# Kernel tuning notes

Hardware: AMD Instinct MI355X
Metric: run time of the kernel (lower is better)

## Reference

```python
import jax, jax.numpy as jnp
import numpy as np

B, C1, C2, H, W, NH = 16, 256, 256, 64, 64, 8
C = C2 // 2          # hidden dim of retention blocks (c2*e)
HD = C // NH         # head dim
EPS = 1e-5           # torch BatchNorm2d / LayerNorm default eps


def _ln(x, g, b):
    mu = jnp.mean(x, -1, keepdims=True)
    var = jnp.mean((x - mu) ** 2, -1, keepdims=True)
    return (x - mu) * jax.lax.rsqrt(var + EPS) * g + b


def _bn_silu(y, g, b, m, v):
    # inference-mode BatchNorm2d (running stats) + SiLU, channels axis=1
    y = (y - m[:, None, None]) * jax.lax.rsqrt(v + EPS)[:, None, None] * g[:, None, None] + b[:, None, None]
    return jax.nn.silu(y)


def _decay1d(L, dec):
    # RelPos2d.generate_1d_decay: exp(decay_n * |i-j|), shape (NH, L, L)
    idx = jnp.arange(L)
    m = jnp.abs(idx[:, None] - idx[None, :]).astype(jnp.float32)
    return jnp.exp(dec[:, None, None] * m)


def setup_inputs() -> dict:
    key = jax.random.key(0)
    ks = jax.random.split(key, 8)
    s = 0.02
    return {
        'x': jax.random.normal(ks[0], (B, C1, H, W), jnp.float32),
        'cv1_w': jax.random.normal(ks[1], (2 * C, C1), jnp.float32) * s,
        'bn1_g': jnp.ones((2 * C,)), 'bn1_b': jnp.zeros((2 * C,)),
        'bn1_m': jnp.zeros((2 * C,)), 'bn1_v': jnp.ones((2 * C,)),
        'cv2_w': jax.random.normal(ks[2], (C2, 3 * C), jnp.float32) * s,
        'bn2_g': jnp.ones((C2,)), 'bn2_b': jnp.zeros((C2,)),
        'bn2_m': jnp.zeros((C2,)), 'bn2_v': jnp.ones((C2,)),
        'ln1_g': jnp.ones((C,)), 'ln1_b': jnp.zeros((C,)),
        'qkv_w': jax.random.normal(ks[3], (3 * C, C), jnp.float32) * s,
        'qkv_b': jnp.zeros((3 * C,)),
        'proj_w': jax.random.normal(ks[4], (C, C), jnp.float32) * s,
        'proj_b': jnp.zeros((C,)),
        'gamma': jnp.ones((C,)),
        'ln2_g': jnp.ones((C,)), 'ln2_b': jnp.zeros((C,)),
        'ffn_w1': jax.random.normal(ks[5], (2 * C, C), jnp.float32) * s,
        'ffn_b1': jnp.zeros((2 * C,)),
        'ffn_w2': jax.random.normal(ks[6], (C, 2 * C), jnp.float32) * s,
        'ffn_b2': jnp.zeros((C,)),
    }


def reference(x, cv1_w, bn1_g, bn1_b, bn1_m, bn1_v, cv2_w, bn2_g, bn2_b, bn2_m, bn2_v,
              ln1_g, ln1_b, qkv_w, qkv_b, proj_w, proj_b, gamma,
              ln2_g, ln2_b, ffn_w1, ffn_b1, ffn_w2, ffn_b2):
    # RelPos2d: decay per head, initial_value=2, heads_range=4; mode='chunk' -> 1D decays
    dec = jnp.log(1.0 - 2.0 ** (-2.0 - 4.0 * jnp.arange(NH, dtype=jnp.float32) / NH))
    decay_h = _decay1d(H, dec)  # (NH, H, H)
    decay_w = _decay1d(W, dec)  # (NH, W, W)

    # cv1: 1x1 conv + BN + SiLU, then chunk into two halves of C channels
    y = _bn_silu(jnp.einsum('bchw,oc->bohw', x, cv1_w), bn1_g, bn1_b, bn1_m, bn1_v)
    y1, y2 = y[:, :C], y[:, C:]

    # RetBlock on channels-last feature map
    f = jnp.transpose(y2, (0, 2, 3, 1))  # (B,H,W,C)
    res = f
    fn = _ln(f, ln1_g, ln1_b)
    qkv = fn @ qkv_w.T + qkv_b
    q, k, v = jnp.split(qkv, 3, axis=-1)

    def heads(t):
        return jnp.transpose(t.reshape(B, H, W, NH, HD), (0, 3, 1, 2, 4))  # (B,NH,H,W,HD)

    q, k, v = heads(q), heads(k), heads(v)

    # axial retention: row attention with exponential row-decay
    qk_h = jnp.einsum('bnhwc,bnHwc->bnhHw', q, k) * decay_h[None, :, :, :, None]
    out_h = jnp.einsum('bnhHw,bnHwc->bnhwc', qk_h, v)
    # column attention with exponential column-decay
    qk_w = jnp.einsum('bnhwc,bnhWc->bnhwW', q, k) * decay_w[None, :, None, :, :]
    out_w = jnp.einsum('bnhwW,bnhWc->bnhwc', qk_w, v)
    out = 0.5 * (out_h + out_w)
    out = jnp.transpose(out, (0, 2, 3, 1, 4)).reshape(B, H, W, C)

    f = res + (out @ proj_w.T + proj_b) * gamma
    res2 = f
    fn2 = _ln(f, ln2_g, ln2_b)
    h1 = jax.nn.gelu(fn2 @ ffn_w1.T + ffn_b1, approximate=False)
    f = res2 + (h1 @ ffn_w2.T + ffn_b2)

    f = jnp.transpose(f, (0, 3, 1, 2))  # back to (B,C,H,W)
    cat = jnp.concatenate([y1, y2, f], axis=1)  # (B,3C,H,W)
    return _bn_silu(jnp.einsum('bchw,oc->bohw', cat, cv2_w), bn2_g, bn2_b, bn2_m, bn2_v)
```

## Files before the change

### kernel.cpp

```cpp
#include <hip/hip_runtime.h>
#include <math.h>

#define LEPS 1e-5f
static constexpr int NPOS = 65536;

typedef __attribute__((ext_vector_type(8))) short short8;
typedef __attribute__((ext_vector_type(4))) float floatx4;

__device__ __forceinline__ ushort f2bf(float f) {
    unsigned int u = __float_as_uint(f);
    u += 0x7FFF + ((u >> 16) & 1);
    return (ushort)(u >> 16);
}
__device__ __forceinline__ float bfu(ushort h) {
    return __uint_as_float((unsigned int)h << 16);
}
__device__ __forceinline__ float bfl(unsigned int u) {
    return __uint_as_float(u << 16);
}
__device__ __forceinline__ float bfh(unsigned int u) {
    return __uint_as_float(u & 0xffff0000u);
}

typedef __attribute__((address_space(1))) const unsigned int gu32_t;
typedef __attribute__((address_space(3))) unsigned int lu32_t;
__device__ __forceinline__ void gld16(const ushort* g, ushort* l) {
    __builtin_amdgcn_global_load_lds((gu32_t*)g, (lu32_t*)l, 16, 0, 0);
}

struct WcvtArgs { const float* src[6]; ushort* dst[6]; int n[6]; };
__global__ __launch_bounds__(256)
void wcvt_k(WcvtArgs a)
{
    const int seg = blockIdx.y;
    const float* s = a.src[seg];
    ushort* d = a.dst[seg];
    const int n = a.n[seg];
    for (int i = blockIdx.x * 256 + threadIdx.x; i < n; i += gridDim.x * 256)
        d[i] = f2bf(s[i]);
}

__global__ __launch_bounds__(256)
void bnprep_k(const float* g1, const float* b1, const float* m1, const float* v1,
              const float* g2, const float* b2, const float* m2, const float* v2,
              float* s1, float* h1, float* s2, float* h2)
{
    const int i = threadIdx.x;
    if (blockIdx.x == 0) {
        const float s = g1[i] * rsqrtf(v1[i] + LEPS);
        s1[i] = s; h1[i] = b1[i] - m1[i] * s;
    } else {
        const float s = g2[i] * rsqrtf(v2[i] + LEPS);
        s2[i] = s; h2[i] = b2[i] - m2[i] * s;
    }
}

__global__ __launch_bounds__(256)
void tr_k(const float* __restrict__ x, ushort* __restrict__ xT)
{
    __shared__ float tile[64][65];
    const int t = threadIdx.x;
    const int bi = blockIdx.x;
    const int hwt = bi & 63, ct = (bi >> 6) & 3, b = bi >> 8;
    const int p0 = b * 4096 + hwt * 64, c0 = ct * 64;
    const float* src = x + ((size_t)(b * 256 + c0) << 12) + hwt * 64;
#pragma unroll
    for (int i = 0; i < 16; i++) {
        int cc = (t >> 6) + i * 4;
        tile[cc][t & 63] = src[((size_t)cc << 12) + (t & 63)];
    }
    __syncthreads();
    const int c2 = (t & 31) * 2;
    const int pr = t >> 5;
#pragma unroll
    for (int i = 0; i < 8; i++) {
        int pp = pr + i * 8;
        unsigned int u = (unsigned int)f2bf(tile[c2][pp])
                       | ((unsigned int)f2bf(tile[c2 + 1][pp]) << 16);
        *(unsigned int*)&xT[(size_t)(p0 + pp) * 256 + c0 + c2] = u;
    }
}

template<int KDIM, int ARS, int AMODE, int EPI, int LN>
__global__ __launch_bounds__(256)
void gemm_k(const ushort* __restrict__ A0, const ushort* __restrict__ A1,
            const ushort* __restrict__ Wm, const float* __restrict__ bias,
            const float* __restrict__ q0, const float* __restrict__ q1,
            const ushort* __restrict__ resh,
            const float* __restrict__ lng, const float* __restrict__ lnb,
            ushort* __restrict__ lnout, void* __restrict__ outv, int ors)
{
    constexpr int NT = KDIM / 64;
    __shared__ __align__(16) ushort smem[4 * 128 * 64];
    const int t = threadIdx.x;
    const int p0 = blockIdx.x * 128;
    const int o0 = blockIdx.y * 128;
    const int lane = t & 63, wv = t >> 6;
    const int wm = (wv & 1) * 64, wn = (wv >> 1) * 64;
    const int ln15 = lane & 15, quad = lane >> 4;
    const int dl_row = lane >> 3;
    const int dl_sch = (lane & 7) ^ dl_row;
    const int c_off0 = ((quad) ^ (ln15 & 7)) * 8;
    const int c_off1 = ((4 + quad) ^ (ln15 & 7)) * 8;
    floatx4 acc[4][4] = {};

    const int a3row = t >> 1, a3half = t & 1;
    uint4 ra[4], rb4[4];

    auto stageA = [&](int k0, int bc) {
#pragma unroll
        for (int i = 0; i < 4; i++) {
            const int r0 = wv * 32 + i * 8;
            const int row = r0 + dl_row;
            const ushort* src;
            if (AMODE == 2) {
                if (k0 < 256) src = A0 + (size_t)(p0 + row) * 256 + k0 + dl_sch * 8;
                else          src = A1 + (size_t)(p0 + row) * 128 + (k0 - 256) + dl_sch * 8;
            } else {
                src = A0 + (size_t)(p0 + row) * ARS + k0 + dl_sch * 8;
            }
            gld16(src, &smem[bc * 8192 + r0 * 64]);
        }
    };
    auto stageB = [&](int k0, int bc) {
#pragma unroll
        for (int i = 0; i < 4; i++) {
            const int r0 = wv * 32 + i * 8;
            gld16(Wm + (size_t)(o0 + r0 + dl_row) * KDIM + k0 + dl_sch * 8,
                  &smem[16384 + bc * 8192 + r0 * 64]);
        }
    };
    auto loadA3 = [&](int k0) {
        const ushort* s1 = A0 + (size_t)(p0 + a3row) * 128 + k0 + a3half * 32;
        const ushort* s2 = A1 + (size_t)(p0 + a3row) * 128 + k0 + a3half * 32;
#pragma unroll
        for (int i = 0; i < 4; i++) { ra[i] = ((const uint4*)s1)[i]; rb4[i] = ((const uint4*)s2)[i]; }
    };
    auto writeA3 = [&](int bc) {
#pragma unroll
        for (int i = 0; i < 4; i++) {
            const unsigned int* ap = (const unsigned int*)&ra[i];
            const unsigned int* bp = (const unsigned int*)&rb4[i];
            uint4 w; unsigned int* wp = (unsigned int*)&w;
#pragma unroll
            for (int j = 0; j < 4; j++)
                wp[j] = (unsigned int)f2bf(0.5f * (bfl(ap[j]) + bfl(bp[j])))
                      | ((unsigned int)f2bf(0.5f * (bfh(ap[j]) + bfh(bp[j]))) << 16);
            const int pch = (a3half * 4 + i) ^ (a3row & 7);
            *(uint4*)&smem[bc * 8192 + a3row * 64 + pch * 8] = w;
        }
    };
    auto compute = [&](int bc) {
#pragma unroll
        for (int kh = 0; kh < 2; kh++) {
            const int co = kh ? c_off1 : c_off0;
            short8 a[4], b[4];
#pragma unroll
            for (int i = 0; i < 4; i++)
                a[i] = *(const short8*)&smem[bc * 8192 + (wm + i * 16 + ln15) * 64 + co];
#pragma unroll
            for (int j = 0; j < 4; j++)
                b[j] = *(const short8*)&smem[16384 + bc * 8192 + (wn + j * 16 + ln15) * 64 + co];
#pragma unroll
            for (int i = 0; i < 4; i++)
#pragma unroll
                for (int j = 0; j < 4; j++)
                    acc[i][j] = __builtin_amdgcn_mfma_f32_16x16x32_bf16(
                        a[i], b[j], acc[i][j], 0, 0, 0);
        }
    };

    if (AMODE == 3) {
        loadA3(0);
        stageB(0, 0);
#pragma unroll
        for (int tt = 0; tt < NT; ++tt) {
            const int cur = tt & 1;
            writeA3(cur);
            if (tt + 1 < NT) {
                loadA3((tt + 1) * 64);
                stageB((tt + 1) * 64, cur ^ 1);
                asm volatile("s_waitcnt vmcnt(12) lgkmcnt(0)" ::: "memory");
            } else {
                asm volatile("s_waitcnt vmcnt(0) lgkmcnt(0)" ::: "memory");
            }
            __builtin_amdgcn_s_barrier();
            __builtin_amdgcn_sched_barrier(0);
            compute(cur);
            __builtin_amdgcn_sched_barrier(0);
            __builtin_amdgcn_s_barrier();
        }
    } else {
        stageA(0, 0); stageB(0, 0);
#pragma unroll
        for (int tt = 0; tt < NT; ++tt) {
            const int cur = tt & 1;
            if (tt + 1 < NT) {
                stageA((tt + 1) * 64, cur ^ 1);
                stageB((tt + 1) * 64, cur ^ 1);
                asm volatile("s_waitcnt vmcnt(8)" ::: "memory");
            } else {
                asm volatile("s_waitcnt vmcnt(0)" ::: "memory");
            }
            __builtin_amdgcn_s_barrier();
            __builtin_amdgcn_sched_barrier(0);
            compute(cur);
            __builtin_amdgcn_sched_barrier(0);
            __builtin_amdgcn_s_barrier();
        }
    }

    if (EPI == 2) {
        float* cb = (float*)smem;
        float* ob = (float*)outv + (((size_t)(p0 >> 12) * 256) << 12);
        const int hw0 = p0 & 4095;
#pragma unroll
        for (int chunk = 0; chunk < 2; chunk++) {
            __syncthreads();
            if ((wn >> 6) == chunk) {
#pragma unroll
                for (int i = 0; i < 4; i++)
#pragma unroll
                for (int j = 0; j < 4; j++) {
                    const int ch = j * 16 + ln15;
                    const int o = o0 + chunk * 64 + ch;
                    const float sc = q0[o], sh = q1[o];
#pragma unroll
                    for (int r = 0; r < 4; r++) {
                        const int pos = wm + i * 16 + quad * 4 + r;
                        float v = acc[i][j][r] * sc + sh;
                        v = v / (1.f + __expf(-v));
                        cb[ch * 132 + pos] = v;
                    }
                }
            }
            __syncthreads();
#pragma unroll
            for (int it = 0; it < 8; it++) {
                const int flat = it * 1024 + t * 4;
                const int ch = flat >> 7, pos = flat & 127;
                const int o = o0 + chunk * 64 + ch;
                float4 v4 = *(const float4*)&cb[ch * 132 + pos];
                *(float4*)&ob[((size_t)o << 12) + hw0 + pos] = v4;
            }
        }
        return;
    }

    const bool lnact = LN && (EPI != 1 || o0 == 128);
    ushort (*lt)[136] = (ushort (*)[136])smem;
#pragma unroll
    for (int i = 0; i < 4; i++) {
#pragma unroll
        for (int r = 0; r < 4; r++) {
            const int lr = wm + i * 16 + quad * 4 + r;
            const int p = p0 + lr;
#pragma unroll
            for (int j = 0; j < 4; j++) {
                const int ol = wn + j * 16 + ln15;
                const int o = o0 + ol;
                float v = acc[i][j][r];
                if (EPI == 0) {
                    v += bias[o];
                } else if (EPI == 1) {
                    v = v * q0[o] + q1[o];
                    v = v / (1.f + __expf(-v));
                } else if (EPI == 4) {
                    v = bfu(resh[(size_t)p * 256 + 128 + o]) + (v + bias[o]) * q0[o];
                }
                lt[lr][ol] = f2bf(v);
            }
        }
    }
    __syncthreads();
    {
        ushort* o16 = (ushort*)outv;
#pragma unroll
        for (int it = 0; it < 8; it++) {
            const int flat = it * 256 + t;
            const int row = flat >> 4, ch = (flat & 15) * 8;
            *(uint4*)&o16[(size_t)(p0 + row) * (size_t)ors + o0 + ch] =
                *(const uint4*)&lt[row][ch];
        }
    }

    if (lnact) {
        const int rrow = t >> 1, rhalf = t & 1;
        const ushort* rp = &lt[rrow][rhalf * 64];
        float s = 0.f, s2 = 0.f;
#pragma unroll
        for (int i = 0; i < 8; i++) {
            const uint4 u = *(const uint4*)(rp + i * 8);
            const unsigned int ww[4] = {u.x, u.y, u.z, u.w};
#pragma unroll
            for (int j = 0; j < 4; j++) {
                const float a = bfl(ww[j]), c = bfh(ww[j]);
                s += a + c; s2 += a * a + c * c;
            }
        }
        s += __shfl_xor(s, 1); s2 += __shfl_xor(s2, 1);
        const float mu = s * (1.f / 128.f);
        const float rn = rsqrtf(s2 * (1.f / 128.f) - mu * mu + LEPS);
        ushort* op = lnout + (size_t)(p0 + rrow) * 128 + rhalf * 64;
#pragma unroll
        for (int i = 0; i < 8; i++) {
            const uint4 u = *(const uint4*)(rp + i * 8);
            const unsigned int ww[4] = {u.x, u.y, u.z, u.w};
            uint4 wout;
            unsigned int* wo = (unsigned int*)&wout;
#pragma unroll
            for (int j = 0; j < 4; j++) {
                const int ch = rhalf * 64 + i * 8 + j * 2;
                const float2 gg = *(const float2*)(lng + ch);
                const float2 bb = *(const float2*)(lnb + ch);
                const float a = (bfl(ww[j]) - mu) * rn * gg.x + bb.x;
                const float c = (bfh(ww[j]) - mu) * rn * gg.y + bb.y;
                wo[j] = (unsigned int)f2bf(a) | ((unsigned int)f2bf(c) << 16);
            }
            *(uint4*)(op + i * 8) = wout;
        }
    }
}

__global__ __launch_bounds__(256)
void ffn_k(const ushort* __restrict__ fn2, const ushort* __restrict__ w1,
           const float* __restrict__ b1, const ushort* __restrict__ w2,
           const float* __restrict__ b2, ushort* __restrict__ f)
{
    __shared__ __align__(16) ushort smem[64 * 64 + 256 * 64 + 64 * 264];
    ushort* Ax = smem;
    ushort* Wt = smem + 64 * 64;
    ushort (*H1)[264] = (ushort (*)[264])(smem + 64 * 64 + 256 * 64);
    const int t = threadIdx.x;
    const int p0 = blockIdx.x * 64;
    const int lane = t & 63, wv = t >> 6;
    const int ln15 = lane & 15, quad = lane >> 4;
    const int dl_row = lane >> 3;
    const int dl_sch = (lane & 7) ^ dl_row;
    const int c_off0 = ((quad) ^ (ln15 & 7)) * 8;
    const int c_off1 = ((4 + quad) ^ (ln15 & 7)) * 8;

    float bb1[4], bb2[2];
#pragma unroll
    for (int j = 0; j < 4; j++) bb1[j] = b1[wv * 64 + j * 16 + ln15];
#pragma unroll
    for (int j = 0; j < 2; j++) bb2[j] = b2[wv * 32 + j * 16 + ln15];

    floatx4 acc1[4][4] = {};
    for (int k0 = 0; k0 < 128; k0 += 64) {
#pragma unroll
        for (int i = 0; i < 2; i++) {
            const int r0 = wv * 16 + i * 8;
            gld16(fn2 + (size_t)(p0 + r0 + dl_row) * 128 + k0 + dl_sch * 8, &Ax[r0 * 64]);
        }
#pragma unroll
        for (int i = 0; i < 8; i++) {
            const int r0 = wv * 64 + i * 8;
            gld16(w1 + (size_t)(r0 + dl_row) * 128 + k0 + dl_sch * 8, &Wt[r0 * 64]);
        }
        __syncthreads();
#pragma unroll
        for (int kh = 0; kh < 2; kh++) {
            const int co = kh ? c_off1 : c_off0;
            short8 a[4], b[4];
#pragma unroll
            for (int i = 0; i < 4; i++)
                a[i] = *(const short8*)&Ax[(i * 16 + ln15) * 64 + co];
#pragma unroll
            for (int j = 0; j < 4; j++)
                b[j] = *(const short8*)&Wt[(wv * 64 + j * 16 + ln15) * 64 + co];
#pragma unroll
            for (int i = 0; i < 4; i++)
#pragma unroll
                for (int j = 0; j < 4; j++)
                    acc1[i][j] = __builtin_amdgcn_mfma_f32_16x16x32_bf16(
                        a[i], b[j], acc1[i][j], 0, 0, 0);
        }
        __syncthreads();
    }
#pragma unroll
    for (int i = 0; i < 4; i++) {
        const int r0 = wv * 32 + i * 8;
        gld16(w2 + (size_t)(r0 + dl_row) * 256 + dl_sch * 8, &Wt[r0 * 64]);
    }
    {
#pragma unroll
        for (int i = 0; i < 4; i++)
#pragma unroll
        for (int j = 0; j < 4; j++)
#pragma unroll
        for (int r = 0; r < 4; r++) {
            float v = acc1[i][j][r] + bb1[j];
            v = 0.5f * v * (1.f + erff(v * 0.70710678118654752f));
            H1[i * 16 + quad * 4 + r][wv * 64 + j * 16 + ln15] = f2bf(v);
        }
    }
    asm volatile("s_waitcnt lgkmcnt(0)" ::: "memory");
    __builtin_amdgcn_s_barrier();
    __builtin_amdgcn_sched_barrier(0);

    floatx4 acc2[4][2] = {};
#pragma unroll
    for (int t4 = 0; t4 < 4; ++t4) {
        const int cur = t4 & 1;
        if (t4 + 1 < 4) {
#pragma unroll
            for (int i = 0; i < 4; i++) {
                const int r0 = wv * 32 + i * 8;
                gld16(w2 + (size_t)(r0 + dl_row) * 256 + (t4 + 1) * 64 + dl_sch * 8,
                      &Wt[(cur ^ 1) * 8192 + r0 * 64]);
            }
            asm volatile("s_waitcnt vmcnt(4)" ::: "memory");
        } else {
#pragma unroll
            for (int i = 0; i < 4; i++) {
                const int r0 = wv * 16 + i * 4;
                gld16(f + (size_t)(p0 + r0 + (lane >> 4)) * 128 + (lane & 15) * 8,
                      &smem[r0 * 128]);
            }
            asm volatile("s_waitcnt vmcnt(4)" ::: "memory");
        }
        __builtin_amdgcn_s_barrier();
        __builtin_amdgcn_sched_barrier(0);
#pragma unroll
        for (int kh = 0; kh < 2; kh++) {
            const int co = kh ? c_off1 : c_off0;
            short8 a[4], b[2];
#pragma unroll
            for (int i = 0; i < 4; i++)
                a[i] = *(const short8*)&H1[i * 16 + ln15][t4 * 64 + kh * 32 + quad * 8];
#pragma unroll
            for (int j = 0; j < 2; j++)
                b[j] = *(const short8*)&Wt[cur * 8192 + (wv * 32 + j * 16 + ln15) * 64 + co];
#pragma unroll
            for (int i = 0; i < 4; i++)
#pragma unroll
                for (int j = 0; j < 2; j++)
                    acc2[i][j] = __builtin_amdgcn_mfma_f32_16x16x32_bf16(
                        a[i], b[j], acc2[i][j], 0, 0, 0);
        }
        __builtin_amdgcn_sched_barrier(0);
        __builtin_amdgcn_s_barrier();
    }
    asm volatile("s_waitcnt vmcnt(0)" ::: "memory");
    __builtin_amdgcn_s_barrier();

    ushort* Ft = smem;
    {
#pragma unroll
        for (int i = 0; i < 4; i++)
#pragma unroll
        for (int r = 0; r < 4; r++) {
            const int pos = i * 16 + quad * 4 + r;
#pragma unroll
            for (int j = 0; j < 2; j++) {
                const int ch = wv * 32 + j * 16 + ln15;
                const int idx = pos * 128 + ch;
                Ft[idx] = f2bf(bfu(Ft[idx]) + acc2[i][j][r] + bb2[j]);
            }
        }
    }
    __syncthreads();
#pragma unroll
    for (int it = 0; it < 4; it++) {
        const int flat = it * 256 + t;
        const int row = flat >> 4, ch = (flat & 15) * 8;
        *(uint4*)&f[(size_t)(p0 + row) * 128 + ch] = *(const uint4*)&Ft[row * 128 + ch];
    }
}

__global__ __launch_bounds__(256)
void attn_k(const ushort* __restrict__ qkv, ushort* __restrict__ oh,
            ushort* __restrict__ ow)
{
    __shared__ ushort VtS[4][16 * 72];
    __shared__ ushort SbS[4][64 * 72];
    __shared__ float dpow[128];
    const int t = threadIdx.x, wv = t >> 6, lane = t & 63;
    const int ln15 = lane & 15, quad = lane >> 4;
    const int dirH = (blockIdx.y == 0);
    ushort* outb = dirH ? oh : ow;
    const int blk = blockIdx.x;
    const int lg = blk & 15, n = (blk >> 4) & 7, b = blk >> 7;
    if (t < 128) {
        const float dec = logf(1.f - exp2f(-2.f - 0.5f * (float)n));
        int d = t - 63; if (d < 0) d = -d;
        dpow[t] = __expf(dec * (float)d);
    }
    const int fixed = lg * 4 + wv;
    const int stride = dirH ? 64 : 1;
    const size_t base = (size_t)b * 4096 + (dirH ? fixed : fixed * 64);
    const size_t cbase = base * 384 + n * 16;

    {
        const ushort* vp = qkv + cbase + (size_t)lane * stride * 384 + 256;
        const uint4 va = *(const uint4*)vp, vb = *(const uint4*)(vp + 8);
        ushort* vt = VtS[wv] + lane;
        const unsigned int w[8] = { va.x, va.y, va.z, va.w, vb.x, vb.y, vb.z, vb.w };
#pragma unroll
        for (int d = 0; d < 8; d++) {
            vt[(2 * d) * 72]     = (ushort)(w[d] & 0xffff);
            vt[(2 * d + 1) * 72] = (ushort)(w[d] >> 16);
        }
    }
    short8 qa[4], kb[4];
    {
        const short8 z = {0, 0, 0, 0, 0, 0, 0, 0};
#pragma unroll
        for (int mt = 0; mt < 4; mt++) {
            const int i = mt * 16 + ln15;
            if (quad < 2) {
                const ushort* qp = qkv + cbase + (size_t)i * stride * 384 + quad * 8;
                qa[mt] = *(const short8*)qp;
                kb[mt] = *(const short8*)(qp + 128);
            } else { qa[mt] = z; kb[mt] = z; }
        }
    }
    __syncthreads();

#pragma unroll
    for (int mt = 0; mt < 4; mt++) {
#pragma unroll
        for (int nt = 0; nt < 4; nt++) {
            floatx4 c = {0.f, 0.f, 0.f, 0.f};
            c = __builtin_amdgcn_mfma_f32_16x16x32_bf16(qa[mt], kb[nt], c, 0, 0, 0);
            const int i0 = mt * 16 + quad * 4;
            const int jl = nt * 16 + ln15;
            const float* lut = dpow + (i0 - jl + 63);
            ushort* sb = SbS[wv] + i0 * 72 + jl;
#pragma unroll
            for (int r = 0; r < 4; r++)
                sb[r * 72] = f2bf(c[r] * lut[r]);
        }
    }
    __syncthreads();

    short8 av[2];
#pragma unroll
    for (int c = 0; c < 2; c++)
        av[c] = *(const short8*)&VtS[wv][ln15 * 72 + c * 32 + quad * 8];
    floatx4 o[4] = {};
#pragma unroll
    for (int nt4 = 0; nt4 < 4; nt4++) {
#pragma unroll
        for (int c = 0; c < 2; c++) {
            const short8 bs = *(const short8*)
                &SbS[wv][(nt4 * 16 + ln15) * 72 + c * 32 + quad * 8];
            o[nt4] = __builtin_amdgcn_mfma_f32_16x16x32_bf16(av[c], bs, o[nt4], 0, 0, 0);
        }
    }
#pragma unroll
    for (int nt4 = 0; nt4 < 4; nt4++) {
        const int i = nt4 * 16 + ln15;
        ushort* op = outb + (base + (size_t)i * stride) * 128 + n * 16 + quad * 4;
        uint2 w;
        w.x = (unsigned int)f2bf(o[nt4][0]) | ((unsigned int)f2bf(o[nt4][1]) << 16);
        w.y = (unsigned int)f2bf(o[nt4][2]) | ((unsigned int)f2bf(o[nt4][3]) << 16);
        *(uint2*)op = w;
    }
}

extern "C" void kernel_launch(void* const* d_in, const int* in_sizes, int n_in,
                              void* d_out, int out_size, void* d_ws, size_t ws_size,
                              hipStream_t stream)
{
    const float* x      = (const float*)d_in[0];
    const float* cv1_w  = (const float*)d_in[1];
    const float* bn1_g  = (const float*)d_in[2];
    const float* bn1_b  = (const float*)d_in[3];
    const float* bn1_m  = (const float*)d_in[4];
    const float* bn1_v  = (const float*)d_in[5];
    const float* cv2_w  = (const float*)d_in[6];
    const float* bn2_g  = (const float*)d_in[7];
    const float* bn2_b  = (const float*)d_in[8];
    const float* bn2_m  = (const float*)d_in[9];
    const float* bn2_v  = (const float*)d_in[10];
    const float* ln1_g  = (const float*)d_in[11];
    const float* ln1_b  = (const float*)d_in[12];
    const float* qkv_w  = (const float*)d_in[13];
    const float* qkv_b  = (const float*)d_in[14];
    const float* proj_w = (const float*)d_in[15];
    const float* proj_b = (const float*)d_in[16];
    const float* gamma  = (const float*)d_in[17];
    const float* ln2_g  = (const float*)d_in[18];
    const float* ln2_b  = (const float*)d_in[19];
    const float* ffn_w1 = (const float*)d_in[20];
    const float* ffn_b1 = (const float*)d_in[21];
    const float* ffn_w2 = (const float*)d_in[22];
    const float* ffn_b2 = (const float*)d_in[23];

    ushort* W = (ushort*)d_ws;
    ushort* y    = W;
    ushort* f    = y    + (size_t)NPOS * 256;
    ushort* tmp  = f    + (size_t)NPOS * 128;
    ushort* owb  = tmp  + (size_t)NPOS * 128;
    ushort* qkvb = owb  + (size_t)NPOS * 128;
    ushort* xT   = qkvb + (size_t)NPOS * 384;
    ushort* wc1  = xT   + (size_t)NPOS * 256;
    ushort* wqkv = wc1  + 65536;
    ushort* wpr  = wqkv + 49152;
    ushort* ww1  = wpr  + 16384;
    ushort* ww2  = ww1  + 32768;
    ushort* wc2  = ww2  + 32768;
    float*  bns1 = (float*)(wc2 + 98304);
    float*  bnb1 = bns1 + 256;
    float*  bns2 = bnb1 + 256;
    float*  bnb2 = bns2 + 256;
    float*  out  = (float*)d_out;

    WcvtArgs wa;
    wa.src[0] = cv1_w;  wa.dst[0] = wc1;  wa.n[0] = 65536;
    wa.src[1] = qkv_w;  wa.dst[1] = wqkv; wa.n[1] = 49152;
    wa.src[2] = proj_w; wa.dst[2] = wpr;  wa.n[2] = 16384;
    wa.src[3] = ffn_w1; wa.dst[3] = ww1;  wa.n[3] = 32768;
    wa.src[4] = ffn_w2; wa.dst[4] = ww2;  wa.n[4] = 32768;
    wa.src[5] = cv2_w;  wa.dst[5] = wc2;  wa.n[5] = 98304;
    wcvt_k<<<dim3(96, 6), 256, 0, stream>>>(wa);
    bnprep_k<<<2, 256, 0, stream>>>(bn1_g, bn1_b, bn1_m, bn1_v,
                                    bn2_g, bn2_b, bn2_m, bn2_v,
                                    bns1, bnb1, bns2, bnb2);
    tr_k<<<4096, 256, 0, stream>>>(x, xT);

    gemm_k<256, 256, 0, 1, 1><<<dim3(512, 2), 256, 0, stream>>>(
        xT, nullptr, wc1, nullptr, bns1, bnb1, nullptr, ln1_g, ln1_b, tmp, y, 256);
    gemm_k<128, 128, 0, 0, 0><<<dim3(512, 3), 256, 0, stream>>>(
        tmp, nullptr, wqkv, qkv_b, nullptr, nullptr, nullptr, nullptr, nullptr,
        nullptr, qkvb, 384);
    attn_k<<<dim3(2048, 2), 256, 0, stream>>>(qkvb, tmp, owb);
    gemm_k<128, 128, 3, 4, 1><<<dim3(512, 1), 256, 0, stream>>>(
        tmp, owb, wpr, proj_b, gamma, nullptr, y, ln2_g, ln2_b, tmp, f, 128);
    ffn_k<<<1024, 256, 0, stream>>>(tmp, ww1, ffn_b1, ww2, ffn_b2, f);
    gemm_k<384, 0, 2, 2, 0><<<dim3(512, 2), 256, 0, stream>>>(
        y, f, wc2, nullptr, bns2, bnb2, nullptr, nullptr, nullptr, nullptr, out, 0);
}
```

Before: 338.5 us.

## Halve GEMM K-tile and split epilogue into two halves to shrink LDS

Drops the GEMM K-step from 64 to 32, which shrinks the double-buffered LDS tiles from 64 KB to about 33 KB. The XOR swizzle is reworked for the 32-wide rows, and the vmcnt waits are adjusted to match. The epilogue now stages the 128x128 output tile in two 64-row halves, so its staging buffer fits inside the smaller LDS allocation. The aim is higher occupancy from lower LDS use, at the cost of twice as many barrier-separated K iterations and extra epilogue syncs.

```diff
diff --git a/kernel.cpp b/kernel.cpp
--- a/kernel.cpp
+++ b/kernel.cpp
@@ -90,27 +90,28 @@
             const float* __restrict__ lng, const float* __restrict__ lnb,
             ushort* __restrict__ lnout, void* __restrict__ outv, int ors)
 {
-    constexpr int NT = KDIM / 64;
-    __shared__ __align__(16) ushort smem[4 * 128 * 64];
+    constexpr int NT = KDIM / 32;
+    __shared__ __align__(16) ushort smem[16896];
     const int t = threadIdx.x;
     const int p0 = blockIdx.x * 128;
     const int o0 = blockIdx.y * 128;
     const int lane = t & 63, wv = t >> 6;
     const int wm = (wv & 1) * 64, wn = (wv >> 1) * 64;
     const int ln15 = lane & 15, quad = lane >> 4;
-    const int dl_row = lane >> 3;
-    const int dl_sch = (lane & 7) ^ dl_row;
-    const int c_off0 = ((quad) ^ (ln15 & 7)) * 8;
-    const int c_off1 = ((4 + quad) ^ (ln15 & 7)) * 8;
+    const int dl_row = lane >> 2;
+    const int dl_sch = (lane & 3) ^ (dl_row & 3) ^ ((dl_row >> 2) & 3);
+    const int sfr = (ln15 & 3) ^ ((ln15 >> 2) & 3);
+    const int c_off = (quad ^ sfr) * 8;
     floatx4 acc[4][4] = {};
 
     const int a3row = t >> 1, a3half = t & 1;
-    uint4 ra[4], rb4[4];
+    const int a3s = (a3row & 3) ^ ((a3row >> 2) & 3);
+    uint4 ra[2], rb4[2];
 
     auto stageA = [&](int k0, int bc) {
 #pragma unroll
-        for (int i = 0; i < 4; i++) {
-            const int r0 = wv * 32 + i * 8;
+        for (int i = 0; i < 2; i++) {
+            const int r0 = wv * 32 + i * 16;
             const int row = r0 + dl_row;
             const ushort* src;
             if (AMODE == 2) {
@@ -119,26 +120,26 @@
             } else {
                 src = A0 + (size_t)(p0 + row) * ARS + k0 + dl_sch * 8;
             }
-            gld16(src, &smem[bc * 8192 + r0 * 64]);
+            gld16(src, &smem[bc * 4096 + r0 * 32]);
         }
     };
     auto stageB = [&](int k0, int bc) {
 #pragma unroll
-        for (int i = 0; i < 4; i++) {
-            const int r0 = wv * 32 + i * 8;
+        for (int i = 0; i < 2; i++) {
+            const int r0 = wv * 32 + i * 16;
             gld16(Wm + (size_t)(o0 + r0 + dl_row) * KDIM + k0 + dl_sch * 8,
-                  &smem[16384 + bc * 8192 + r0 * 64]);
+                  &smem[8192 + bc * 4096 + r0 * 32]);
         }
     };
     auto loadA3 = [&](int k0) {
-        const ushort* s1 = A0 + (size_t)(p0 + a3row) * 128 + k0 + a3half * 32;
-        const ushort* s2 = A1 + (size_t)(p0 + a3row) * 128 + k0 + a3half * 32;
-#pragma unroll
-        for (int i = 0; i < 4; i++) { ra[i] = ((const uint4*)s1)[i]; rb4[i] = ((const uint4*)s2)[i]; }
+        const ushort* s1 = A0 + (size_t)(p0 + a3row) * 128 + k0 + a3half * 16;
+        const ushort* s2 = A1 + (size_t)(p0 + a3row) * 128 + k0 + a3half * 16;
+#pragma unroll
+        for (int i = 0; i < 2; i++) { ra[i] = ((const uint4*)s1)[i]; rb4[i] = ((const uint4*)s2)[i]; }
     };
     auto writeA3 = [&](int bc) {
 #pragma unroll
-        for (int i = 0; i < 4; i++) {
+        for (int i = 0; i < 2; i++) {
             const unsigned int* ap = (const unsigned int*)&ra[i];
             const unsigned int* bp = (const unsigned int*)&rb4[i];
             uint4 w; unsigned int* wp = (unsigned int*)&w;
@@ -146,28 +147,24 @@
             for (int j = 0; j < 4; j++)
                 wp[j] = (unsigned int)f2bf(0.5f * (bfl(ap[j]) + bfl(bp[j])))
                       | ((unsigned int)f2bf(0.5f * (bfh(ap[j]) + bfh(bp[j]))) << 16);
-            const int pch = (a3half * 4 + i) ^ (a3row & 7);
-            *(uint4*)&smem[bc * 8192 + a3row * 64 + pch * 8] = w;
+            const int pch = (a3half * 2 + i) ^ a3s;
+            *(uint4*)&smem[bc * 4096 + a3row * 32 + pch * 8] = w;
         }
     };
     auto compute = [&](int bc) {
-#pragma unroll
-        for (int kh = 0; kh < 2; kh++) {
-            const int co = kh ? c_off1 : c_off0;
-            short8 a[4], b[4];
-#pragma unroll
-            for (int i = 0; i < 4; i++)
-                a[i] = *(const short8*)&smem[bc * 8192 + (wm + i * 16 + ln15) * 64 + co];
+        short8 a[4], b[4];
+#pragma unroll
+        for (int i = 0; i < 4; i++)
+            a[i] = *(const short8*)&smem[bc * 4096 + (wm + i * 16 + ln15) * 32 + c_off];
+#pragma unroll
+        for (int j = 0; j < 4; j++)
+            b[j] = *(const short8*)&smem[8192 + bc * 4096 + (wn + j * 16 + ln15) * 32 + c_off];
+#pragma unroll
+        for (int i = 0; i < 4; i++)
 #pragma unroll
             for (int j = 0; j < 4; j++)
-                b[j] = *(const short8*)&smem[16384 + bc * 8192 + (wn + j * 16 + ln15) * 64 + co];
-#pragma unroll
-            for (int i = 0; i < 4; i++)
-#pragma unroll
-                for (int j = 0; j < 4; j++)
-                    acc[i][j] = __builtin_amdgcn_mfma_f32_16x16x32_bf16(
-                        a[i], b[j], acc[i][j], 0, 0, 0);
-        }
+                acc[i][j] = __builtin_amdgcn_mfma_f32_16x16x32_bf16(
+                    a[i], b[j], acc[i][j], 0, 0, 0);
     };
 
     if (AMODE == 3) {
@@ -178,9 +175,9 @@
             const int cur = tt & 1;
             writeA3(cur);
             if (tt + 1 < NT) {
-                loadA3((tt + 1) * 64);
-                stageB((tt + 1) * 64, cur ^ 1);
-                asm volatile("s_waitcnt vmcnt(12) lgkmcnt(0)" ::: "memory");
+                loadA3((tt + 1) * 32);
+                stageB((tt + 1) * 32, cur ^ 1);
+                asm volatile("s_waitcnt vmcnt(6) lgkmcnt(0)" ::: "memory");
             } else {
                 asm volatile("s_waitcnt vmcnt(0) lgkmcnt(0)" ::: "memory");
             }
@@ -196,9 +193,9 @@
         for (int tt = 0; tt < NT; ++tt) {
             const int cur = tt & 1;
             if (tt + 1 < NT) {
-                stageA((tt + 1) * 64, cur ^ 1);
-                stageB((tt + 1) * 64, cur ^ 1);
-                asm volatile("s_waitcnt vmcnt(8)" ::: "memory");
+                stageA((tt + 1) * 32, cur ^ 1);
+                stageB((tt + 1) * 32, cur ^ 1);
+                asm volatile("s_waitcnt vmcnt(4)" ::: "memory");
             } else {
                 asm volatile("s_waitcnt vmcnt(0)" ::: "memory");
             }
@@ -249,76 +246,79 @@
 
     const bool lnact = LN && (EPI != 1 || o0 == 128);
     ushort (*lt)[136] = (ushort (*)[136])smem;
-#pragma unroll
-    for (int i = 0; i < 4; i++) {
-#pragma unroll
-        for (int r = 0; r < 4; r++) {
-            const int lr = wm + i * 16 + quad * 4 + r;
-            const int p = p0 + lr;
-#pragma unroll
-            for (int j = 0; j < 4; j++) {
-                const int ol = wn + j * 16 + ln15;
-                const int o = o0 + ol;
-                float v = acc[i][j][r];
-                if (EPI == 0) {
-                    v += bias[o];
-                } else if (EPI == 1) {
-                    v = v * q0[o] + q1[o];
-                    v = v / (1.f + __expf(-v));
-                } else if (EPI == 4) {
-                    v = bfu(resh[(size_t)p * 256 + 128 + o]) + (v + bias[o]) * q0[o];
+    ushort* o16 = (ushort*)outv;
+#pragma unroll
+    for (int ck = 0; ck < 2; ck++) {
+        if ((wv & 1) == ck) {
+#pragma unroll
+            for (int i = 0; i < 4; i++) {
+#pragma unroll
+                for (int r = 0; r < 4; r++) {
+                    const int lr = i * 16 + quad * 4 + r;
+                    const int p = p0 + ck * 64 + lr;
+#pragma unroll
+                    for (int j = 0; j < 4; j++) {
+                        const int ol = wn + j * 16 + ln15;
+                        const int o = o0 + ol;
+                        float v = acc[i][j][r];
+                        if (EPI == 0) {
+                            v += bias[o];
+                        } else if (EPI == 1) {
+                            v = v * q0[o] + q1[o];
+                            v = v / (1.f + __expf(-v));
+                        } else if (EPI == 4) {
+                            v = bfu(resh[(size_t)p * 256 + 128 + o]) + (v + bias[o]) * q0[o];
+                        }
+                        lt[lr][ol] = f2bf(v);
+                    }
                 }
-                lt[lr][ol] = f2bf(v);
-            }
-        }
-    }
-    __syncthreads();
-    {
-        ushort* o16 = (ushort*)outv;
-#pragma unroll
-        for (int it = 0; it < 8; it++) {
+            }
+        }
+        __syncthreads();
+#pragma unroll
+        for (int it = 0; it < 4; it++) {
             const int flat = it * 256 + t;
-            const int row = flat >> 4, ch = (flat & 15) * 8;
-            *(uint4*)&o16[(size_t)(p0 + row) * (size_t)ors + o0 + ch] =
-                *(const uint4*)&lt[row][ch];
-        }
-    }
-
-    if (lnact) {
-        const int rrow = t >> 1, rhalf = t & 1;
-        const ushort* rp = &lt[rrow][rhalf * 64];
-        float s = 0.f, s2 = 0.f;
-#pragma unroll
-        for (int i = 0; i < 8; i++) {
-            const uint4 u = *(const uint4*)(rp + i * 8);
-            const unsigned int ww[4] = {u.x, u.y, u.z, u.w};
-#pragma unroll
-            for (int j = 0; j < 4; j++) {
-                const float a = bfl(ww[j]), c = bfh(ww[j]);
-                s += a + c; s2 += a * a + c * c;
-            }
-        }
-        s += __shfl_xor(s, 1); s2 += __shfl_xor(s2, 1);
-        const float mu = s * (1.f / 128.f);
-        const float rn = rsqrtf(s2 * (1.f / 128.f) - mu * mu + LEPS);
-        ushort* op = lnout + (size_t)(p0 + rrow) * 128 + rhalf * 64;
-#pragma unroll
-        for (int i = 0; i < 8; i++) {
-            const uint4 u = *(const uint4*)(rp + i * 8);
-            const unsigned int ww[4] = {u.x, u.y, u.z, u.w};
-            uint4 wout;
-            unsigned int* wo = (unsigned int*)&wout;
-#pragma unroll
-            for (int j = 0; j < 4; j++) {
-                const int ch = rhalf * 64 + i * 8 + j * 2;
-                const float2 gg = *(const float2*)(lng + ch);
-                const float2 bb = *(const float2*)(lnb + ch);
-                const float a = (bfl(ww[j]) - mu) * rn * gg.x + bb.x;
-                const float c = (bfh(ww[j]) - mu) * rn * gg.y + bb.y;
-                wo[j] = (unsigned int)f2bf(a) | ((unsigned int)f2bf(c) << 16);
-            }
-            *(uint4*)(op + i * 8) = wout;
-        }
+            const int row = flat >> 4, ch8 = (flat & 15) * 8;
+            *(uint4*)&o16[(size_t)(p0 + ck * 64 + row) * (size_t)ors + o0 + ch8] =
+                *(const uint4*)&lt[row][ch8];
+        }
+        if (lnact && t < 128) {
+            const int rrow = t >> 1, rhalf = t & 1;
+            const ushort* rp = &lt[rrow][rhalf * 64];
+            float s = 0.f, s2 = 0.f;
+#pragma unroll
+            for (int i = 0; i < 8; i++) {
+                const uint4 u = *(const uint4*)(rp + i * 8);
+                const unsigned int ww[4] = {u.x, u.y, u.z, u.w};
+#pragma unroll
+                for (int j = 0; j < 4; j++) {
+                    const float a = bfl(ww[j]), c = bfh(ww[j]);
+                    s += a + c; s2 += a * a + c * c;
+                }
+            }
+            s += __shfl_xor(s, 1); s2 += __shfl_xor(s2, 1);
+            const float mu = s * (1.f / 128.f);
+            const float rn = rsqrtf(s2 * (1.f / 128.f) - mu * mu + LEPS);
+            ushort* op = lnout + (size_t)(p0 + ck * 64 + rrow) * 128 + rhalf * 64;
+#pragma unroll
+            for (int i = 0; i < 8; i++) {
+                const uint4 u = *(const uint4*)(rp + i * 8);
+                const unsigned int ww[4] = {u.x, u.y, u.z, u.w};
+                uint4 wout;
+                unsigned int* wo = (unsigned int*)&wout;
+#pragma unroll
+                for (int j = 0; j < 4; j++) {
+                    const int ch = rhalf * 64 + i * 8 + j * 2;
+                    const float2 gg = *(const float2*)(lng + ch);
+                    const float2 bb = *(const float2*)(lnb + ch);
+                    const float a = (bfl(ww[j]) - mu) * rn * gg.x + bb.x;
+                    const float c = (bfh(ww[j]) - mu) * rn * gg.y + bb.y;
+                    wo[j] = (unsigned int)f2bf(a) | ((unsigned int)f2bf(c) << 16);
+                }
+                *(uint4*)(op + i * 8) = wout;
+            }
+        }
+        __syncthreads();
     }
 }
 
```

Measured after the change: 357.6 us. +5.7%, slower.
